# Optimization experiments

Hardware: AMD Instinct MI355X
Metric: run time of the kernel (lower is better)

Reference implementation:

```python
import jax, jax.numpy as jnp
import numpy as np

B, S, D, K, L, H = 2, 2048, 1024, 256, 2, 16
HD = D // H
F = 4 * D
EPS = 1e-5
NEG = -1e30


def setup_inputs() -> dict:
    key = jax.random.key(0)
    ks = jax.random.split(key, 20)
    # ragged segment boundaries: sorted, last boundary pinned to S-1 so the
    # expanded sequence is exactly seq_len long (required for torch.stack)
    boundaries = jnp.sort(jax.random.randint(ks[0], (B, K), 0, S - 1), axis=1)
    boundaries = boundaries.at[:, -1].set(S - 1).astype(jnp.int32)
    counts = jnp.full((B,), K, dtype=jnp.int32)
    x_processed = jax.random.normal(ks[1], (B, K, D), jnp.float32) * 0.02
    x_residual = jax.random.normal(ks[2], (B, S, D), jnp.float32) * 0.02
    # RoPE tables [S, HD]
    inv_freq = 1.0 / (10000.0 ** (jnp.arange(0, HD, 2, dtype=jnp.float32) / HD))
    freqs = jnp.outer(jnp.arange(S, dtype=jnp.float32), inv_freq)
    emb = jnp.concatenate([freqs, freqs], axis=-1)
    cos, sin = jnp.cos(emb), jnp.sin(emb)
    sc = D ** -0.5
    params = dict(
        start_emb=jax.random.normal(ks[3], (D,), jnp.float32) * 0.02,
        Wq=jax.random.normal(ks[4], (L, D, D)) * sc,
        Wk=jax.random.normal(ks[5], (L, D, D)) * sc,
        Wv=jax.random.normal(ks[6], (L, D, D)) * sc,
        Wo=jax.random.normal(ks[7], (L, D, D)) * sc,
        Wg=jax.random.normal(ks[8], (L, D, F)) * sc,
        Wu=jax.random.normal(ks[9], (L, D, F)) * sc,
        Wd=jax.random.normal(ks[10], (L, F, D)) * (F ** -0.5),
        ln1=jnp.ones((L, D), jnp.float32),
        ln2=jnp.ones((L, D), jnp.float32),
        fnorm=jnp.ones((D,), jnp.float32),
    )
    return dict(x_processed=x_processed, boundaries=boundaries, counts=counts,
                x_residual=x_residual, cos=cos, sin=sin, seq_len=S, **params)


def _rms(x, w):
    return x * jax.lax.rsqrt(jnp.mean(x * x, axis=-1, keepdims=True) + EPS) * w


def _rope(x, cos, sin):
    # x: [B, H, S, HD]; cos/sin: [S, HD]
    x1, x2 = jnp.split(x, 2, axis=-1)
    rot = jnp.concatenate([-x2, x1], axis=-1)
    return x * cos[None, None] + rot * sin[None, None]


def reference(x_processed, boundaries, counts, x_residual, cos, sin, seq_len,
              start_emb, Wq, Wk, Wv, Wo, Wg, Wu, Wd, ln1, ln2, fnorm):
    b, k, d = x_processed.shape
    # --- vectorized ragged repeat-expand ---
    # position t belongs to segment i iff boundaries[i-1] < t <= boundaries[i]
    t = jnp.arange(seq_len)
    valid = jnp.arange(k)[None, :] < counts[:, None]
    bnd = jnp.where(valid, boundaries, seq_len)          # mask out unused slots
    seg = jax.vmap(lambda bb: jnp.searchsorted(bb, t, side='left'))(bnd)  # [B,S]
    # segment 0 -> start_emb, segment i>0 -> x_processed[:, i-1]
    reps = jnp.concatenate(
        [jnp.broadcast_to(start_emb, (b, 1, d)), x_processed], axis=1)  # [B,K+1,D]
    x = jnp.take_along_axis(reps, seg[..., None], axis=1) + x_residual

    causal = jnp.tril(jnp.ones((seq_len, seq_len), bool))
    scale = HD ** -0.5
    for l in range(L):
        h = _rms(x, ln1[l])
        q = (h @ Wq[l]).reshape(b, seq_len, H, HD).transpose(0, 2, 1, 3)
        kk = (h @ Wk[l]).reshape(b, seq_len, H, HD).transpose(0, 2, 1, 3)
        v = (h @ Wv[l]).reshape(b, seq_len, H, HD).transpose(0, 2, 1, 3)
        q, kk = _rope(q, cos, sin), _rope(kk, cos, sin)
        att = jnp.einsum('bhqd,bhkd->bhqk', q, kk) * scale
        att = jax.nn.softmax(jnp.where(causal, att, NEG), axis=-1)
        o = jnp.einsum('bhqk,bhkd->bhqd', att, v)
        o = o.transpose(0, 2, 1, 3).reshape(b, seq_len, d)
        x = x + o @ Wo[l]
        h = _rms(x, ln2[l])
        x = x + (jax.nn.silu(h @ Wg[l]) * (h @ Wu[l])) @ Wd[l]
    return _rms(x, fnorm)
```

## Files before the change

### kernel.cpp

```cpp
#include <hip/hip_runtime.h>
#include <hip/hip_bf16.h>

#define S_LEN  2048
#define NB     2
#define DIM    1024
#define KSEG   256
#define NLAYER 2
#define NHEAD  16
#define HDIM   64
#define FDIM   4096
#define NROW   (NB * S_LEN)

typedef __bf16 bf16x8 __attribute__((ext_vector_type(8)));
typedef float  f32x4  __attribute__((ext_vector_type(4)));
typedef __hip_bfloat16 bf16_t;

struct __align__(8)  us4 { unsigned short v[4]; };
struct __align__(16) us8 { unsigned short v[8]; };

__device__ __forceinline__ unsigned short f2bf(float f) {
  __hip_bfloat16 t = __float2bfloat16(f);
  return __builtin_bit_cast(unsigned short, t);
}
__device__ __forceinline__ float bf2f(unsigned short x) {
  return __bfloat162float(__builtin_bit_cast(__hip_bfloat16, x));
}

__device__ __forceinline__ void gload_lds16(const void* g, void* l) {
  __builtin_amdgcn_global_load_lds((__attribute__((address_space(1))) void*)g,
                                   (__attribute__((address_space(3))) void*)l,
                                   16, 0, 0);
}

__device__ __forceinline__ f32x4 mfma16(bf16x8 a, bf16x8 b, f32x4 c) {
  return __builtin_amdgcn_mfma_f32_16x16x32_bf16(a, b, c, 0, 0, 0);
}

__device__ __forceinline__ bf16_t* swz(bf16_t* base, int r, int kElem) {
  int byte = ((r << 7) + (kElem << 1)) ^ ((r & 7) << 4);
  return (bf16_t*)((char*)base + byte);
}
__device__ __forceinline__ const bf16_t* swz(const bf16_t* base, int r, int kElem) {
  int byte = ((r << 7) + (kElem << 1)) ^ ((r & 7) << 4);
  return (const bf16_t*)((const char*)base + byte);
}

__global__ __launch_bounds__(256) void expand_kernel(
    const float* __restrict__ xp, const int* __restrict__ bnd,
    const int* __restrict__ counts, const float* __restrict__ xres,
    const float* __restrict__ semb, float* __restrict__ x) {
  const int bt = blockIdx.x;
  const int b = bt >> 11, t = bt & (S_LEN - 1);
  const int cnt = counts[b];
  const int* bb = bnd + b * KSEG;
  int lo = 0, hi = KSEG;
  while (lo < hi) {
    int mid = (lo + hi) >> 1;
    int v = (mid < cnt) ? bb[mid] : S_LEN;
    if (v < t) lo = mid + 1; else hi = mid;
  }
  const float* src = (lo == 0) ? semb : (xp + ((size_t)b * KSEG + (lo - 1)) * DIM);
  const int tid = threadIdx.x;
  float4 a = ((const float4*)src)[tid];
  float4 r = ((const float4*)(xres + (size_t)bt * DIM))[tid];
  float4 w; w.x = a.x + r.x; w.y = a.y + r.y; w.z = a.z + r.z; w.w = a.w + r.w;
  ((float4*)(x + (size_t)bt * DIM))[tid] = w;
}

template <int F32OUT>
__global__ __launch_bounds__(256) void rmsnorm_kernel(
    const float* __restrict__ x, const float* __restrict__ wgt,
    bf16_t* __restrict__ ob, float* __restrict__ of) {
  const int row = blockIdx.x, tid = threadIdx.x;
  const float4 v = ((const float4*)(x + (size_t)row * DIM))[tid];
  float ss = v.x * v.x + v.y * v.y + v.z * v.z + v.w * v.w;
#pragma unroll
  for (int off = 1; off < 64; off <<= 1) ss += __shfl_xor(ss, off);
  __shared__ float red[4];
  if ((tid & 63) == 0) red[tid >> 6] = ss;
  __syncthreads();
  ss = red[0] + red[1] + red[2] + red[3];
  const float r = rsqrtf(ss * (1.0f / DIM) + 1e-5f);
  const float4 wv = ((const float4*)wgt)[tid];
  if (F32OUT) {
    float4 o4; o4.x = v.x * r * wv.x; o4.y = v.y * r * wv.y;
    o4.z = v.z * r * wv.z; o4.w = v.w * r * wv.w;
    ((float4*)(of + (size_t)row * DIM))[tid] = o4;
  } else {
    us4 p;
    p.v[0] = f2bf(v.x * r * wv.x); p.v[1] = f2bf(v.y * r * wv.y);
    p.v[2] = f2bf(v.z * r * wv.z); p.v[3] = f2bf(v.w * r * wv.w);
    ((us4*)(ob + (size_t)row * DIM))[tid] = p;
  }
}

template <int MODE>
__global__ __launch_bounds__(256) void transpose_cast(
    const float* __restrict__ in, bf16_t* __restrict__ out, int R, int C) {
  __shared__ float tile[32][33];
  const int tx = threadIdx.x & 31, ty = threadIdx.x >> 5;
  const int cb = blockIdx.x * 32, rb = blockIdx.y * 32;
#pragma unroll
  for (int i = 0; i < 4; i++) {
    int r = ty + i * 8;
    tile[r][tx] = in[(size_t)(rb + r) * C + cb + tx];
  }
  __syncthreads();
#pragma unroll
  for (int i = 0; i < 4; i++) {
    int r = ty + i * 8;
    int n = cb + r;
    int dr = (MODE == 0) ? n : (((n >> 4) << 5) + (n & 15) + (MODE == 2 ? 16 : 0));
    out[(size_t)dr * R + rb + tx] = __float2bfloat16(tile[tx][r]);
  }
}

template <int FUSE>
__global__ __launch_bounds__(512, 2) void gemm_bt256(
    const bf16_t* __restrict__ A, const bf16_t* __restrict__ Bt,
    bf16_t* __restrict__ C, int ldc, int K, int lda, int nbn, int nbm) {
  __shared__ __align__(16) bf16_t As[2][256][64];
  __shared__ __align__(16) bf16_t Bs[2][256][64];
  const int bid = blockIdx.x;
  const int bmC = nbm >> 1, bnC = nbn >> 2;
  const int c8 = bid & 7, idx = bid >> 3;
  const int bm = (c8 & 1) * bmC + idx / bnC;
  const int bn = (c8 >> 1) * bnC + idx % bnC;
  const int tid = threadIdx.x;
  const int lane = tid & 63, w = tid >> 6;
  const int wm = w >> 2, wn = w & 3;
  const int l15 = lane & 15, l16 = lane >> 4;
  const bf16_t* Ag = A + (size_t)bm * 256 * lda;
  const bf16_t* Bg = Bt + (size_t)bn * 256 * K;
  const int NT = K >> 6;

  f32x4 acc[8][4] = {};

  auto stage = [&](int j) {
    const int t = j >> 2, item = j & 3, buf = t & 1;
    bf16_t* dst;
    const bf16_t* src;
    int stride;
    if (item < 2) { dst = &Bs[buf][item * 128][0];
                    src = Bg + (size_t)item * 128 * K;  stride = K;   }
    else          { dst = &As[buf][(item - 2) * 128][0];
                    src = Ag + (size_t)(item - 2) * 128 * lda; stride = lda; }
    const int k0 = t << 6;
#pragma unroll
    for (int i = 0; i < 2; i++) {
      int c = i * 512 + tid;
      int row = c >> 3, q = c & 7;
      int colE = (q ^ (row & 7)) << 3;
      gload_lds16(src + (size_t)row * stride + k0 + colE, dst + c * 8);
    }
  };
  auto frag = [&](const bf16_t* tile, int row, int kk) -> bf16x8 {
    int byte = ((row << 7) + (kk << 6) + (l16 << 4)) ^ ((row & 7) << 4);
    return *(const bf16x8*)((const char*)tile + byte);
  };

  for (int j = 0; j < 7; j++) stage(j);
  asm volatile("s_waitcnt vmcnt(6)" ::: "memory");
  __builtin_amdgcn_s_barrier();

  for (int t = 0; t < NT; t++) {
    const int buf = t & 1;
    const bf16_t* At = &As[buf][0][0];
    const bf16_t* Bc = &Bs[buf][0][0];
    bf16x8 bfrg[4][2];
    const int jb = (t << 2) + 7;
#pragma unroll
    for (int p = 0; p < 4; p++) {
      bf16x8 afrg[2][2];
      if (p == 0) {
#pragma unroll
        for (int ni = 0; ni < 4; ni++)
#pragma unroll
          for (int kk = 0; kk < 2; kk++)
            bfrg[ni][kk] = frag(Bc, wn * 64 + ni * 16 + l15, kk);
      }
#pragma unroll
      for (int mi = 0; mi < 2; mi++)
#pragma unroll
        for (int kk = 0; kk < 2; kk++)
          afrg[mi][kk] = frag(At, wm * 128 + p * 32 + mi * 16 + l15, kk);
      if (jb + p < 4 * NT) stage(jb + p);
      __builtin_amdgcn_sched_barrier(0);
      __builtin_amdgcn_s_barrier();
      asm volatile("s_waitcnt lgkmcnt(0)" ::: "memory");
      __builtin_amdgcn_sched_barrier(0);
      __builtin_amdgcn_s_setprio(1);
#pragma unroll
      for (int mi = 0; mi < 2; mi++)
#pragma unroll
        for (int ni = 0; ni < 4; ni++)
#pragma unroll
          for (int kk = 0; kk < 2; kk++)
            acc[p * 2 + mi][ni] = mfma16(afrg[mi][kk], bfrg[ni][kk],
                                         acc[p * 2 + mi][ni]);
      __builtin_amdgcn_s_setprio(0);
      __builtin_amdgcn_sched_barrier(0);
      if (p == 3) {
        if (t < NT - 2) { asm volatile("s_waitcnt vmcnt(6)" ::: "memory"); }
        else            { asm volatile("s_waitcnt vmcnt(0)" ::: "memory"); }
      }
      __builtin_amdgcn_s_barrier();
    }
  }

  const int r0 = bm * 256 + wm * 128 + (l16 << 2);
  if (FUSE == 0) {
    const int c0 = bn * 256 + wn * 64 + l15;
#pragma unroll
    for (int mi = 0; mi < 8; mi++)
#pragma unroll
      for (int ni = 0; ni < 4; ni++)
#pragma unroll
        for (int r = 0; r < 4; r++)
          C[(size_t)(r0 + mi * 16 + r) * ldc + c0 + ni * 16] =
              __float2bfloat16(acc[mi][ni][r]);
  } else {
    const int c0 = bn * 128 + wn * 32 + l15;
#pragma unroll
    for (int mi = 0; mi < 8; mi++)
#pragma unroll
      for (int j = 0; j < 2; j++)
#pragma unroll
        for (int r = 0; r < 4; r++) {
          float g = acc[mi][2 * j][r], u = acc[mi][2 * j + 1][r];
          float a = g / (1.f + __expf(-g)) * u;
          C[(size_t)(r0 + mi * 16 + r) * ldc + c0 + j * 16] = __float2bfloat16(a);
        }
  }
}

template <int EPI>
__global__ __launch_bounds__(256) void gemm_sn(
    const bf16_t* __restrict__ A, const bf16_t* __restrict__ Bt,
    bf16_t* __restrict__ Cb, float* __restrict__ Cf, int N, int K, int lda) {
  __shared__ __align__(16) bf16_t As[3][128][64];
  __shared__ __align__(16) bf16_t Bs[3][64][64];
  const int nbn = N >> 6;
  const int bid = blockIdx.x;
  const int sbid = (bid & 7) * (gridDim.x >> 3) + (bid >> 3);
  const int bn = sbid % nbn, bm = sbid / nbn;
  const int tid = threadIdx.x, lane = tid & 63, w = tid >> 6;
  const int wm = w >> 1, wn = w & 1;
  const int l15 = lane & 15, l16 = lane >> 4;
  const bf16_t* Ag = A + (size_t)bm * 128 * lda;
  const bf16_t* Bg = Bt + (size_t)bn * 64 * K;
  f32x4 acc[4][2] = {};
  const int NT = K >> 6;

  auto stage = [&](int buf, int t) {
    const int k0 = t << 6;
#pragma unroll
    for (int i = 0; i < 4; i++) {
      int c = i * 256 + tid;
      int row = c >> 3, q = c & 7;
      int colE = (q ^ (row & 7)) << 3;
      gload_lds16(Ag + (size_t)row * lda + k0 + colE, &As[buf][0][0] + c * 8);
    }
#pragma unroll
    for (int i = 0; i < 2; i++) {
      int c = i * 256 + tid;
      int row = c >> 3, q = c & 7;
      int colE = (q ^ (row & 7)) << 3;
      gload_lds16(Bg + (size_t)row * K + k0 + colE, &Bs[buf][0][0] + c * 8);
    }
  };
  auto frag = [&](const bf16_t* base, int row, int kk) -> bf16x8 {
    int byte = ((row << 7) + (kk << 6) + (l16 << 4)) ^ ((row & 7) << 4);
    return *(const bf16x8*)((const char*)base + byte);
  };

  stage(0, 0);
  if (NT > 1) stage(1, 1);
  int bi = 0;
  for (int t = 0; t < NT; t++) {
    if (t + 1 < NT) { asm volatile("s_waitcnt vmcnt(6)" ::: "memory"); }
    else            { asm volatile("s_waitcnt vmcnt(0)" ::: "memory"); }
    __builtin_amdgcn_s_barrier();
    __builtin_amdgcn_sched_barrier(0);
    if (t + 2 < NT) {
      int nb = bi + 2; if (nb >= 3) nb -= 3;
      stage(nb, t + 2);
    }
    __builtin_amdgcn_sched_barrier(0);
    const bf16_t* Ab = &As[bi][0][0];
    const bf16_t* Bb = &Bs[bi][0][0];
    bf16x8 af[4][2], bfr[2][2];
#pragma unroll
    for (int mi = 0; mi < 4; mi++)
#pragma unroll
      for (int kk = 0; kk < 2; kk++)
        af[mi][kk] = frag(Ab, wm * 64 + mi * 16 + l15, kk);
#pragma unroll
    for (int ni = 0; ni < 2; ni++)
#pragma unroll
      for (int kk = 0; kk < 2; kk++)
        bfr[ni][kk] = frag(Bb, wn * 32 + ni * 16 + l15, kk);
    __builtin_amdgcn_s_setprio(1);
#pragma unroll
    for (int mi = 0; mi < 4; mi++)
#pragma unroll
      for (int ni = 0; ni < 2; ni++)
#pragma unroll
        for (int kk = 0; kk < 2; kk++)
          acc[mi][ni] = mfma16(af[mi][kk], bfr[ni][kk], acc[mi][ni]);
    __builtin_amdgcn_s_setprio(0);
    __builtin_amdgcn_sched_barrier(0);
    bi++; if (bi >= 3) bi -= 3;
  }

  const int r0 = bm * 128 + wm * 64 + (l16 << 2);
  const int c0 = bn * 64 + wn * 32 + l15;
#pragma unroll
  for (int mi = 0; mi < 4; mi++)
#pragma unroll
    for (int ni = 0; ni < 2; ni++)
#pragma unroll
      for (int r = 0; r < 4; r++) {
        size_t off = (size_t)(r0 + mi * 16 + r) * N + c0 + ni * 16;
        if (EPI == 0) Cb[off] = __float2bfloat16(acc[mi][ni][r]);
        else          Cf[off] += acc[mi][ni][r];
      }
}

__global__ __launch_bounds__(256) void rope_kernel(
    bf16_t* __restrict__ qkv, const float* __restrict__ cosb,
    const float* __restrict__ sinb) {
  int idx = blockIdx.x * 256 + threadIdx.x;
  const int i = idx & 31; idx >>= 5;
  const int h = idx & 15; idx >>= 4;
  const int qk = idx & 1; idx >>= 1;
  const int t = idx & (S_LEN - 1); idx >>= 11;
  const int b = idx;
  bf16_t* p = qkv + ((size_t)(b * S_LEN + t)) * 3072 + qk * DIM + h * HDIM;
  const float c = cosb[t * HDIM + i], s = sinb[t * HDIM + i];
  const float x1 = __bfloat162float(p[i]), x2 = __bfloat162float(p[i + 32]);
  p[i]      = __float2bfloat16(x1 * c - x2 * s);
  p[i + 32] = __float2bfloat16(x2 * c + x1 * s);
}

__global__ __launch_bounds__(256) void vtrans_kernel(
    const bf16_t* __restrict__ qkv, bf16_t* __restrict__ vT) {
  const int gid = blockIdx.x;
  const int tb = gid & 31, bh = gid >> 5;
  const int b = bh >> 4, h = bh & 15;
  __shared__ bf16_t tile[64][65];
  const int tx = threadIdx.x, ty = threadIdx.y;
  const bf16_t* src = qkv + ((size_t)(b * S_LEN + tb * 64)) * 3072 + 2048 + h * HDIM;
#pragma unroll
  for (int j = 0; j < 16; j++)
    tile[j * 4 + ty][tx] = src[(size_t)(j * 4 + ty) * 3072 + tx];
  __syncthreads();
  bf16_t* dst = vT + ((size_t)bh * 64) * S_LEN + tb * 64;
#pragma unroll
  for (int j = 0; j < 16; j++) {
    int d = j * 4 + ty;
    dst[(size_t)d * S_LEN + tx] = tile[tx][d];
  }
}

__global__ __launch_bounds__(256) void attn_kernel(
    const bf16_t* __restrict__ qkv, const bf16_t* __restrict__ vT,
    bf16_t* __restrict__ o) {
  __shared__ __align__(16) bf16_t Ks[3][64][64];
  __shared__ __align__(16) bf16_t Vs[3][64][64];
  __shared__ __align__(16) bf16_t Ps[64][64];
  const int bid = blockIdx.x;
  const int pair = (bid >> 3) & 15;
  const int bh = (bid & 7) + ((bid >> 7) << 3);
  const int b = bh >> 4, h = bh & 15;
  const int tid = threadIdx.x, lane = tid & 63, w = tid >> 6;
  const int l15 = lane & 15;
  const int kq = (lane >> 4) << 3;
  const int rq = (lane >> 4) << 2;
  const bf16_t* kbase = qkv + (size_t)b * S_LEN * 3072 + 1024 + h * HDIM;
  const bf16_t* vbase = vT + ((size_t)bh * 64) * S_LEN;

  bf16x8 ones;
#pragma unroll
  for (int e = 0; e < 8; e++) ones[e] = (__bf16)1.0f;

#define STAGE(buf, kt) do {                                                    \
    const bf16_t* kg_ = kbase + (size_t)(kt) * 64 * 3072;                      \
    const bf16_t* vg_ = vbase + (kt) * 64;                                     \
    _Pragma("unroll")                                                          \
    for (int i_ = 0; i_ < 2; i_++) {                                           \
      int cb_ = i_ * 256 + w * 64;                                             \
      int c_ = cb_ + lane;                                                     \
      int row_ = c_ >> 3;                                                      \
      int colE_ = ((c_ & 7) ^ (row_ & 7)) << 3;                                \
      gload_lds16(kg_ + (size_t)row_ * 3072 + colE_,                           \
                  &Ks[buf][0][0] + (size_t)cb_ * 8);                           \
      gload_lds16(vg_ + (size_t)row_ * S_LEN + colE_,                          \
                  &Vs[buf][0][0] + (size_t)cb_ * 8);                           \
    }                                                                          \
  } while (0)

  for (int ph = 0; ph < 2; ph++) {
    const int qb = (ph == 0) ? pair : (31 - pair);
    const int nk = qb + 1;
    const int qrow = qb * 64 + w * 16 + l15;
    const bf16_t* qg = qkv + ((size_t)(b * S_LEN + qrow)) * 3072 + h * HDIM;
    bf16x8 aq0 = *(const bf16x8*)(qg + kq);
    bf16x8 aq1 = *(const bf16x8*)(qg + 32 + kq);
    const float qsc = 0.125f * 1.44269504088896340736f;
#pragma unroll
    for (int e = 0; e < 8; e++) {
      aq0[e] = (__bf16)((float)aq0[e] * qsc);
      aq1[e] = (__bf16)((float)aq1[e] * qsc);
    }
    f32x4 oacc[4] = {};
    f32x4 lacc = {0.f, 0.f, 0.f, 0.f};
    float m_r[4];
#pragma unroll
    for (int r = 0; r < 4; r++) m_r[r] = -1e30f;
    const int myrow = qb * 64 + w * 16 + rq;

    __builtin_amdgcn_s_barrier();
    STAGE(0, 0);
    if (nk > 1) STAGE(1, 1);
    int bi = 0;
    for (int kt = 0; kt < nk; kt++) {
      if (kt + 1 < nk) { asm volatile("s_waitcnt vmcnt(4)" ::: "memory"); }
      else             { asm volatile("s_waitcnt vmcnt(0)" ::: "memory"); }
      __builtin_amdgcn_s_barrier();
      __builtin_amdgcn_sched_barrier(0);
      if (kt + 2 < nk) {
        int nb = bi + 2; if (nb >= 3) nb -= 3;
        STAGE(nb, kt + 2);
      }
      __builtin_amdgcn_sched_barrier(0);
      const bf16_t* Kc = &Ks[bi][0][0];
      const bf16_t* Vc = &Vs[bi][0][0];
      f32x4 s[4];
      __builtin_amdgcn_s_setprio(1);
#pragma unroll
      for (int f = 0; f < 4; f++) {
        bf16x8 bk0 = *(const bf16x8*)swz(Kc, f * 16 + l15, kq);
        bf16x8 bk1 = *(const bf16x8*)swz(Kc, f * 16 + l15, 32 + kq);
        f32x4 t = {};
        t = mfma16(aq0, bk0, t);
        t = mfma16(aq1, bk1, t);
        s[f] = t;
      }
      __builtin_amdgcn_s_setprio(0);
      if (kt == qb) {
#pragma unroll
        for (int f = 0; f < 4; f++) {
          int colg = kt * 64 + f * 16 + l15;
#pragma unroll
          for (int r = 0; r < 4; r++)
            if (colg > myrow + r) s[f][r] = -1e30f;
        }
      }
      float mx[4], alpha[4];
#pragma unroll
      for (int r = 0; r < 4; r++)
        mx[r] = fmaxf(fmaxf(s[0][r], s[1][r]), fmaxf(s[2][r], s[3][r]));
#pragma unroll
      for (int r = 0; r < 4; r++) {
#pragma unroll
        for (int off = 1; off < 16; off <<= 1)
          mx[r] = fmaxf(mx[r], __shfl_xor(mx[r], off));
        float mn = fmaxf(m_r[r], mx[r]);
        alpha[r] = exp2f(m_r[r] - mn);
        m_r[r] = mn;
      }
#pragma unroll
      for (int f = 0; f < 4; f++)
#pragma unroll
        for (int r = 0; r < 4; r++)
          s[f][r] = exp2f(s[f][r] - m_r[r]);
#pragma unroll
      for (int ni = 0; ni < 4; ni++)
#pragma unroll
        for (int r = 0; r < 4; r++) oacc[ni][r] *= alpha[r];
#pragma unroll
      for (int r = 0; r < 4; r++) lacc[r] *= alpha[r];
#pragma unroll
      for (int f = 0; f < 4; f++)
#pragma unroll
        for (int r = 0; r < 4; r++)
          *swz(&Ps[0][0], w * 16 + rq + r, f * 16 + l15) = __float2bfloat16(s[f][r]);
      __builtin_amdgcn_s_setprio(1);
#pragma unroll
      for (int kk2 = 0; kk2 < 2; kk2++) {
        bf16x8 ap = *(const bf16x8*)swz(&Ps[0][0], w * 16 + l15, kk2 * 32 + kq);
        lacc = mfma16(ap, ones, lacc);
#pragma unroll
        for (int ni = 0; ni < 4; ni++) {
          bf16x8 bv = *(const bf16x8*)swz(Vc, ni * 16 + l15, kk2 * 32 + kq);
          oacc[ni] = mfma16(ap, bv, oacc[ni]);
        }
      }
      __builtin_amdgcn_s_setprio(0);
      __builtin_amdgcn_sched_barrier(0);
      bi++; if (bi >= 3) bi -= 3;
    }
    bf16_t* ob = o + ((size_t)(b * S_LEN + qb * 64 + w * 16 + rq)) * DIM + h * HDIM + l15;
#pragma unroll
    for (int r = 0; r < 4; r++) {
      float inv = 1.0f / lacc[r];
#pragma unroll
      for (int ni = 0; ni < 4; ni++)
        ob[(size_t)r * DIM + ni * 16] = __float2bfloat16(oacc[ni][r] * inv);
    }
  }
#undef STAGE
}

extern "C" void kernel_launch(void* const* d_in, const int* in_sizes, int n_in,
                              void* d_out, int out_size, void* d_ws, size_t ws_size,
                              hipStream_t stream) {
  (void)in_sizes; (void)n_in; (void)out_size; (void)ws_size;
  const float* x_processed = (const float*)d_in[0];
  const int*   boundaries  = (const int*)d_in[1];
  const int*   counts      = (const int*)d_in[2];
  const float* x_residual  = (const float*)d_in[3];
  const float* cos_t       = (const float*)d_in[4];
  const float* sin_t       = (const float*)d_in[5];
  const float* start_emb   = (const float*)d_in[7];
  const float* Wq  = (const float*)d_in[8];
  const float* Wk  = (const float*)d_in[9];
  const float* Wv  = (const float*)d_in[10];
  const float* Wo  = (const float*)d_in[11];
  const float* Wg  = (const float*)d_in[12];
  const float* Wu  = (const float*)d_in[13];
  const float* Wd  = (const float*)d_in[14];
  const float* ln1 = (const float*)d_in[15];
  const float* ln2 = (const float*)d_in[16];
  const float* fnm = (const float*)d_in[17];

  char* ws = (char*)d_ws;
  const size_t MB = (size_t)1 << 20;
  float*  x      = (float*)(ws);
  bf16_t* h      = (bf16_t*)(ws + 16 * MB);
  bf16_t* Wqkv_t = (bf16_t*)(ws + 24 * MB);
  bf16_t* Wo_t   = (bf16_t*)(ws + 30 * MB);
  bf16_t* Wgu_t  = (bf16_t*)(ws + 32 * MB);
  bf16_t* Wd_t   = (bf16_t*)(ws + 48 * MB);
  char*   Rg     = ws + 56 * MB;
  bf16_t* qkv  = (bf16_t*)(Rg);
  bf16_t* vT   = (bf16_t*)(Rg + 24 * MB);
  bf16_t* obuf = (bf16_t*)(Rg + 32 * MB);
  bf16_t* act  = (bf16_t*)(Rg);

  expand_kernel<<<NROW, 256, 0, stream>>>(x_processed, boundaries, counts,
                                          x_residual, start_emb, x);

  const size_t dd = (size_t)DIM * DIM, df = (size_t)DIM * FDIM;
  for (int l = 0; l < NLAYER; l++) {
    transpose_cast<0><<<dim3(DIM / 32, DIM / 32), 256, 0, stream>>>(Wq + l * dd, Wqkv_t, DIM, DIM);
    transpose_cast<0><<<dim3(DIM / 32, DIM / 32), 256, 0, stream>>>(Wk + l * dd, Wqkv_t + dd, DIM, DIM);
    transpose_cast<0><<<dim3(DIM / 32, DIM / 32), 256, 0, stream>>>(Wv + l * dd, Wqkv_t + 2 * dd, DIM, DIM);
    transpose_cast<0><<<dim3(DIM / 32, DIM / 32), 256, 0, stream>>>(Wo + l * dd, Wo_t, DIM, DIM);
    transpose_cast<1><<<dim3(FDIM / 32, DIM / 32), 256, 0, stream>>>(Wg + l * df, Wgu_t, DIM, FDIM);
    transpose_cast<2><<<dim3(FDIM / 32, DIM / 32), 256, 0, stream>>>(Wu + l * df, Wgu_t, DIM, FDIM);
    transpose_cast<0><<<dim3(DIM / 32, FDIM / 32), 256, 0, stream>>>(Wd + l * df, Wd_t, FDIM, DIM);

    rmsnorm_kernel<0><<<NROW, 256, 0, stream>>>(x, ln1 + l * DIM, h, nullptr);
    gemm_bt256<0><<<(3072 / 256) * (NROW / 256), 512, 0, stream>>>(
        h, Wqkv_t, qkv, 3072, DIM, DIM, 3072 / 256, NROW / 256);
    rope_kernel<<<(NROW * 2 * NHEAD * 32) / 256, 256, 0, stream>>>(qkv, cos_t, sin_t);
    vtrans_kernel<<<NB * NHEAD * (S_LEN / 64), dim3(64, 4), 0, stream>>>(qkv, vT);
    attn_kernel<<<512, 256, 0, stream>>>(qkv, vT, obuf);
    gemm_sn<1><<<(DIM / 64) * (NROW / 128), 256, 0, stream>>>(
        obuf, Wo_t, nullptr, x, DIM, DIM, DIM);

    rmsnorm_kernel<0><<<NROW, 256, 0, stream>>>(x, ln2 + l * DIM, h, nullptr);
    gemm_bt256<1><<<(2 * FDIM / 256) * (NROW / 256), 512, 0, stream>>>(
        h, Wgu_t, act, FDIM, DIM, DIM, 2 * FDIM / 256, NROW / 256);
    gemm_sn<1><<<(DIM / 64) * (NROW / 128), 256, 0, stream>>>(
        act, Wd_t, nullptr, x, DIM, FDIM, FDIM);
  }
  rmsnorm_kernel<1><<<NROW, 256, 0, stream>>>(x, fnm, nullptr, (float*)d_out);
}
```

Before: 629.6 us.

## Fuse RoPE into QKV GEMM epilogue and transpose attention score layout

Applies rotary embedding directly in the QKV GEMM epilogue for Q and K column blocks (bn < 8), removing the separate rope kernel and its read-modify-write pass over Q/K. In attention, the QK^T MFMA operands are swapped so each lane holds scores for one query row. The row max then needs only two cross-lane shuffles, and P is written to LDS as packed 4-element stores instead of scalar stores. The cost is that the alpha rescale factors must be redistributed with per-row shuffles, and cos/sin are now loaded from global memory inside the GEMM epilogue.

```diff
diff --git a/kernel.cpp b/kernel.cpp
--- a/kernel.cpp
+++ b/kernel.cpp
@@ -118,7 +118,8 @@
 template <int FUSE>
 __global__ __launch_bounds__(512, 2) void gemm_bt256(
     const bf16_t* __restrict__ A, const bf16_t* __restrict__ Bt,
-    bf16_t* __restrict__ C, int ldc, int K, int lda, int nbn, int nbm) {
+    bf16_t* __restrict__ C, int ldc, int K, int lda, int nbn, int nbm,
+    const float* __restrict__ cosb, const float* __restrict__ sinb) {
   __shared__ __align__(16) bf16_t As[2][256][64];
   __shared__ __align__(16) bf16_t Bs[2][256][64];
   const int bid = blockIdx.x;
@@ -219,7 +220,7 @@
         for (int r = 0; r < 4; r++)
           C[(size_t)(r0 + mi * 16 + r) * ldc + c0 + ni * 16] =
               __float2bfloat16(acc[mi][ni][r]);
-  } else {
+  } else if (FUSE == 1) {
     const int c0 = bn * 128 + wn * 32 + l15;
 #pragma unroll
     for (int mi = 0; mi < 8; mi++)
@@ -231,6 +232,37 @@
           float a = g / (1.f + __expf(-g)) * u;
           C[(size_t)(r0 + mi * 16 + r) * ldc + c0 + j * 16] = __float2bfloat16(a);
         }
+  } else {
+    const int c0 = bn * 256 + wn * 64 + l15;
+    if (bn < 8) {
+#pragma unroll
+      for (int mi = 0; mi < 8; mi++)
+#pragma unroll
+        for (int r = 0; r < 4; r++) {
+          const int row = r0 + mi * 16 + r;
+          const int tt = row & (S_LEN - 1);
+#pragma unroll
+          for (int ni = 0; ni < 2; ni++) {
+            const int i = ni * 16 + l15;
+            const float cz = cosb[tt * HDIM + i];
+            const float sz = sinb[tt * HDIM + i];
+            const float x1 = acc[mi][ni][r], x2 = acc[mi][ni + 2][r];
+            C[(size_t)row * ldc + c0 + ni * 16] =
+                __float2bfloat16(x1 * cz - x2 * sz);
+            C[(size_t)row * ldc + c0 + (ni + 2) * 16] =
+                __float2bfloat16(x2 * cz + x1 * sz);
+          }
+        }
+    } else {
+#pragma unroll
+      for (int mi = 0; mi < 8; mi++)
+#pragma unroll
+        for (int ni = 0; ni < 4; ni++)
+#pragma unroll
+          for (int r = 0; r < 4; r++)
+            C[(size_t)(r0 + mi * 16 + r) * ldc + c0 + ni * 16] =
+                __float2bfloat16(acc[mi][ni][r]);
+    }
   }
 }
 
@@ -327,22 +359,6 @@
       }
 }
 
-__global__ __launch_bounds__(256) void rope_kernel(
-    bf16_t* __restrict__ qkv, const float* __restrict__ cosb,
-    const float* __restrict__ sinb) {
-  int idx = blockIdx.x * 256 + threadIdx.x;
-  const int i = idx & 31; idx >>= 5;
-  const int h = idx & 15; idx >>= 4;
-  const int qk = idx & 1; idx >>= 1;
-  const int t = idx & (S_LEN - 1); idx >>= 11;
-  const int b = idx;
-  bf16_t* p = qkv + ((size_t)(b * S_LEN + t)) * 3072 + qk * DIM + h * HDIM;
-  const float c = cosb[t * HDIM + i], s = sinb[t * HDIM + i];
-  const float x1 = __bfloat162float(p[i]), x2 = __bfloat162float(p[i + 32]);
-  p[i]      = __float2bfloat16(x1 * c - x2 * s);
-  p[i + 32] = __float2bfloat16(x2 * c + x1 * s);
-}
-
 __global__ __launch_bounds__(256) void vtrans_kernel(
     const bf16_t* __restrict__ qkv, bf16_t* __restrict__ vT) {
   const int gid = blockIdx.x;
@@ -415,10 +431,8 @@
     }
     f32x4 oacc[4] = {};
     f32x4 lacc = {0.f, 0.f, 0.f, 0.f};
-    float m_r[4];
-#pragma unroll
-    for (int r = 0; r < 4; r++) m_r[r] = -1e30f;
-    const int myrow = qb * 64 + w * 16 + rq;
+    float m_s = -1e30f;
+    const int myq = qb * 64 + w * 16 + l15;
 
     __builtin_amdgcn_s_barrier();
     STAGE(0, 0);
@@ -436,56 +450,57 @@
       __builtin_amdgcn_sched_barrier(0);
       const bf16_t* Kc = &Ks[bi][0][0];
       const bf16_t* Vc = &Vs[bi][0][0];
-      f32x4 s[4];
+      f32x4 st[4];
       __builtin_amdgcn_s_setprio(1);
 #pragma unroll
       for (int f = 0; f < 4; f++) {
         bf16x8 bk0 = *(const bf16x8*)swz(Kc, f * 16 + l15, kq);
         bf16x8 bk1 = *(const bf16x8*)swz(Kc, f * 16 + l15, 32 + kq);
         f32x4 t = {};
-        t = mfma16(aq0, bk0, t);
-        t = mfma16(aq1, bk1, t);
-        s[f] = t;
+        t = mfma16(bk0, aq0, t);
+        t = mfma16(bk1, aq1, t);
+        st[f] = t;
       }
       __builtin_amdgcn_s_setprio(0);
       if (kt == qb) {
 #pragma unroll
         for (int f = 0; f < 4; f++) {
-          int colg = kt * 64 + f * 16 + l15;
+          int kvb = kt * 64 + f * 16 + rq;
 #pragma unroll
           for (int r = 0; r < 4; r++)
-            if (colg > myrow + r) s[f][r] = -1e30f;
+            if (kvb + r > myq) st[f][r] = -1e30f;
         }
       }
-      float mx[4], alpha[4];
-#pragma unroll
-      for (int r = 0; r < 4; r++)
-        mx[r] = fmaxf(fmaxf(s[0][r], s[1][r]), fmaxf(s[2][r], s[3][r]));
-#pragma unroll
-      for (int r = 0; r < 4; r++) {
-#pragma unroll
-        for (int off = 1; off < 16; off <<= 1)
-          mx[r] = fmaxf(mx[r], __shfl_xor(mx[r], off));
-        float mn = fmaxf(m_r[r], mx[r]);
-        alpha[r] = exp2f(m_r[r] - mn);
-        m_r[r] = mn;
-      }
+      float mx = -1e30f;
 #pragma unroll
       for (int f = 0; f < 4; f++)
 #pragma unroll
-        for (int r = 0; r < 4; r++)
-          s[f][r] = exp2f(s[f][r] - m_r[r]);
+        for (int r = 0; r < 4; r++) mx = fmaxf(mx, st[f][r]);
+      mx = fmaxf(mx, __shfl_xor(mx, 16));
+      mx = fmaxf(mx, __shfl_xor(mx, 32));
+      const float mn = fmaxf(m_s, mx);
+      const float alpha = exp2f(m_s - mn);
+      m_s = mn;
+#pragma unroll
+      for (int f = 0; f < 4; f++)
+#pragma unroll
+        for (int r = 0; r < 4; r++) st[f][r] = exp2f(st[f][r] - mn);
+      float alpr[4];
+#pragma unroll
+      for (int r = 0; r < 4; r++) alpr[r] = __shfl(alpha, rq + r);
 #pragma unroll
       for (int ni = 0; ni < 4; ni++)
 #pragma unroll
-        for (int r = 0; r < 4; r++) oacc[ni][r] *= alpha[r];
-#pragma unroll
-      for (int r = 0; r < 4; r++) lacc[r] *= alpha[r];
-#pragma unroll
-      for (int f = 0; f < 4; f++)
-#pragma unroll
-        for (int r = 0; r < 4; r++)
-          *swz(&Ps[0][0], w * 16 + rq + r, f * 16 + l15) = __float2bfloat16(s[f][r]);
+        for (int r = 0; r < 4; r++) oacc[ni][r] *= alpr[r];
+#pragma unroll
+      for (int r = 0; r < 4; r++) lacc[r] *= alpr[r];
+#pragma unroll
+      for (int f = 0; f < 4; f++) {
+        us4 pk;
+#pragma unroll
+        for (int r = 0; r < 4; r++) pk.v[r] = f2bf(st[f][r]);
+        *(us4*)swz(&Ps[0][0], w * 16 + l15, f * 16 + rq) = pk;
+      }
       __builtin_amdgcn_s_setprio(1);
 #pragma unroll
       for (int kk2 = 0; kk2 < 2; kk2++) {
@@ -563,9 +578,8 @@
     transpose_cast<0><<<dim3(DIM / 32, FDIM / 32), 256, 0, stream>>>(Wd + l * df, Wd_t, FDIM, DIM);
 
     rmsnorm_kernel<0><<<NROW, 256, 0, stream>>>(x, ln1 + l * DIM, h, nullptr);
-    gemm_bt256<0><<<(3072 / 256) * (NROW / 256), 512, 0, stream>>>(
-        h, Wqkv_t, qkv, 3072, DIM, DIM, 3072 / 256, NROW / 256);
-    rope_kernel<<<(NROW * 2 * NHEAD * 32) / 256, 256, 0, stream>>>(qkv, cos_t, sin_t);
+    gemm_bt256<2><<<(3072 / 256) * (NROW / 256), 512, 0, stream>>>(
+        h, Wqkv_t, qkv, 3072, DIM, DIM, 3072 / 256, NROW / 256, cos_t, sin_t);
     vtrans_kernel<<<NB * NHEAD * (S_LEN / 64), dim3(64, 4), 0, stream>>>(qkv, vT);
     attn_kernel<<<512, 256, 0, stream>>>(qkv, vT, obuf);
     gemm_sn<1><<<(DIM / 64) * (NROW / 128), 256, 0, stream>>>(
@@ -573,7 +587,7 @@
 
     rmsnorm_kernel<0><<<NROW, 256, 0, stream>>>(x, ln2 + l * DIM, h, nullptr);
     gemm_bt256<1><<<(2 * FDIM / 256) * (NROW / 256), 512, 0, stream>>>(
-        h, Wgu_t, act, FDIM, DIM, DIM, 2 * FDIM / 256, NROW / 256);
+        h, Wgu_t, act, FDIM, DIM, DIM, 2 * FDIM / 256, NROW / 256, nullptr, nullptr);
     gemm_sn<1><<<(DIM / 64) * (NROW / 128), 256, 0, stream>>>(
         act, Wd_t, nullptr, x, DIM, FDIM, FDIM);
   }
```

New measurement: 589.9 us (median of 2 runs). -6.3%, faster.
